# Kernel tuning notes

Hardware: AMD Instinct MI355X
Metric: run time of the kernel (lower is better)

## Reference

```python
import jax, jax.numpy as jnp
import numpy as np

NEG_SLOPE = 0.2  # PyG GATConv default leaky_relu slope


def _gat_layer(h, mask, W, att_src, att_dst, bias, concat):
    """PyG-style GATConv (eval mode, add_self_loops handled via mask diag).
    h: [B,N,D_in], mask: [B,N,N] bool (mask[b,i,j]=True if edge j->i, incl. self loop)
    W: [D_in, H*C], att_src/att_dst: [H,C], bias: [H*C] or [C].
    """
    B, N, _ = h.shape
    H, C = att_src.shape
    x = (h @ W).reshape(B, N, H, C)                       # [B,N,H,C]
    e_src = jnp.einsum('bnhc,hc->bnh', x, att_src)        # score contrib of source j
    e_dst = jnp.einsum('bnhc,hc->bnh', x, att_dst)        # score contrib of target i
    # scores[b,i,j,h] = leaky_relu(e_dst_i + e_src_j)
    s = jax.nn.leaky_relu(e_dst[:, :, None, :] + e_src[:, None, :, :], NEG_SLOPE)
    s = jnp.where(mask[..., None], s, -jnp.inf)
    alpha = jax.nn.softmax(s, axis=2)                     # softmax over neighbors j
    out = jnp.einsum('bijh,bjhc->bihc', alpha, x)         # aggregate
    out = out.reshape(B, N, H * C) if concat else out.mean(axis=2)
    return out + bias


def setup_inputs() -> dict:
    key = jax.random.key(0)
    ks = jax.random.split(key, 16)
    B, T, N, F_in = 4, 8, 2000, 158
    D, H = 128, 4
    C = D // H  # 32
    x_alpha = jax.random.normal(ks[0], (B, T, N, F_in), dtype=jnp.float32)
    sector_graph = (jax.random.uniform(ks[1], (B, N, N)) > 0.98).astype(jnp.float32)
    g = lambda k, shp, fan: jax.random.normal(k, shp, dtype=jnp.float32) / np.sqrt(fan)
    return {
        'x_alpha': x_alpha,
        'sector_graph': sector_graph,
        'W_in': g(ks[2], (F_in, D), F_in), 'b_in': jnp.zeros((D,), jnp.float32),
        'ln_g': jnp.ones((D,), jnp.float32), 'ln_b': jnp.zeros((D,), jnp.float32),
        'W0': g(ks[3], (D, H * C), D), 'as0': g(ks[4], (H, C), C), 'ad0': g(ks[5], (H, C), C),
        'bias0': jnp.zeros((H * C,), jnp.float32),
        'W1': g(ks[6], (D, H * C), D), 'as1': g(ks[7], (H, C), C), 'ad1': g(ks[8], (H, C), C),
        'bias1': jnp.zeros((C,), jnp.float32),
        'W_out': g(ks[9], (C, D), C), 'b_out': jnp.zeros((D,), jnp.float32),
    }


def reference(x_alpha, sector_graph, W_in, b_in, ln_g, ln_b,
              W0, as0, ad0, bias0, W1, as1, ad1, bias1, W_out, b_out):
    B, T, N, _ = x_alpha.shape
    x = x_alpha[:, -1]                                    # [B,N,F]
    # input_proj: Linear -> LayerNorm -> ReLU (dropout is identity in eval)
    h = x @ W_in + b_in
    mu = h.mean(-1, keepdims=True)
    var = ((h - mu) ** 2).mean(-1, keepdims=True)
    h = (h - mu) / jnp.sqrt(var + 1e-5) * ln_g + ln_b
    h = jax.nn.relu(h)                                    # [B,N,128]
    # edge mask with self loops (PyG add_self_loops=True)
    eye = jnp.eye(N, dtype=bool)
    mask = (sector_graph > 0) | eye[None]
    # layer 0: concat=True, out dim 128 == in dim -> residual, elu (not last layer)
    h0 = _gat_layer(h, mask, W0, as0, ad0, bias0, concat=True)
    h = h + jax.nn.elu(h0)
    # layer 1 (last): concat=False, out dim 32 != 128 -> no residual, no elu
    h = _gat_layer(h, mask, W1, as1, ad1, bias1, concat=False)  # [B,N,32]
    return h @ W_out + b_out                              # [B,N,128]
```

## Files before the change

kernel.cpp:

```cpp
#include <hip/hip_runtime.h>

typedef unsigned short u16;

__device__ __forceinline__ float us2f(u16 u){
  unsigned int x = ((unsigned int)u) << 16;
  return __uint_as_float(x);
}
__device__ __forceinline__ u16 f2us(float f){
  unsigned int u = __float_as_uint(f);
  unsigned int r = (u + 0x7fffu + ((u >> 16) & 1u)) >> 16;
  return (u16)r;
}
__device__ __forceinline__ float wredSum(float v){
  #pragma unroll
  for (int o = 32; o > 0; o >>= 1) v += __shfl_xor(v, o, 64);
  return v;
}
__device__ __forceinline__ float g32Sum(float v){
  #pragma unroll
  for (int o = 16; o > 0; o >>= 1) v += __shfl_xor(v, o, 32);
  return v;
}
__device__ __forceinline__ float g8Sum(float v){
  #pragma unroll
  for (int o = 4; o > 0; o >>= 1) v += __shfl_xor(v, o, 32);
  return v;
}

#define ACAP 128
#define RBG 32

__global__ __launch_bounds__(256) void k_inln_gat0(
    const float* __restrict__ xA, const float* __restrict__ Win,
    const float* __restrict__ bin, const float* __restrict__ lng,
    const float* __restrict__ lnb, const float* __restrict__ W0,
    const float* __restrict__ as0, const float* __restrict__ ad0,
    float* __restrict__ h, u16* __restrict__ x0,
    float* __restrict__ es, float* __restrict__ ed)
{
  __shared__ float xs[RBG][160];
  __shared__ float Wt[2][8][128];
  const int t = threadIdx.x;
  const int row0 = blockIdx.x * RBG;
  const int tx = t & 31, ty = t >> 5;
  const int c0 = tx * 4, rbase = ty * 4;
  const int wk = ty;

  for (int idx = t; idx < RBG * 160; idx += 256){
    int r = idx / 160, k = idx - r * 160;
    int row = row0 + r;
    int b = row / 2000, n = row - b * 2000;
    xs[r][k] = (k < 158) ? xA[(((size_t)b * 8 + 7) * 2000 + n) * 158 + k] : 0.f;
  }
  *(float4*)&Wt[0][wk][c0] = *(const float4*)&Win[(size_t)wk * 128 + c0];
  __syncthreads();

  float acc[4][4];
  #pragma unroll
  for (int r = 0; r < 4; r++)
    #pragma unroll
    for (int c = 0; c < 4; c++) acc[r][c] = 0.f;

  const int NT1 = 20;
  for (int tl = 0; tl < NT1; tl++){
    const int cur = tl & 1;
    float4 wreg = make_float4(0.f, 0.f, 0.f, 0.f);
    const bool hn = (tl + 1 < NT1);
    if (hn){
      int k = (tl + 1) * 8 + wk;
      if (k < 158) wreg = *(const float4*)&Win[(size_t)k * 128 + c0];
    }
    const int k0 = tl * 8;
    #pragma unroll
    for (int kh = 0; kh < 2; kh++){
      float4 a[4];
      #pragma unroll
      for (int r = 0; r < 4; r++) a[r] = *(const float4*)&xs[rbase + r][k0 + kh * 4];
      #pragma unroll
      for (int kk = 0; kk < 4; kk++){
        float4 w = *(const float4*)&Wt[cur][kh * 4 + kk][c0];
        #pragma unroll
        for (int r = 0; r < 4; r++){
          float av = ((const float*)&a[r])[kk];
          acc[r][0] = fmaf(av, w.x, acc[r][0]);
          acc[r][1] = fmaf(av, w.y, acc[r][1]);
          acc[r][2] = fmaf(av, w.z, acc[r][2]);
          acc[r][3] = fmaf(av, w.w, acc[r][3]);
        }
      }
    }
    if (hn) *(float4*)&Wt[cur ^ 1][wk][c0] = wreg;
    __syncthreads();
  }

  {
    float4 bi = *(const float4*)&bin[c0];
    float4 g  = *(const float4*)&lng[c0];
    float4 be = *(const float4*)&lnb[c0];
    #pragma unroll
    for (int r = 0; r < 4; r++){
      float a0 = acc[r][0] + bi.x, a1 = acc[r][1] + bi.y;
      float a2 = acc[r][2] + bi.z, a3 = acc[r][3] + bi.w;
      float s  = g32Sum(a0 + a1 + a2 + a3);
      float sq = g32Sum(a0*a0 + a1*a1 + a2*a2 + a3*a3);
      float mu  = s * (1.f / 128.f);
      float var = sq * (1.f / 128.f) - mu * mu;
      float inv = rsqrtf(var + 1e-5f);
      float v0 = fmaxf((a0 - mu) * inv * g.x + be.x, 0.f);
      float v1 = fmaxf((a1 - mu) * inv * g.y + be.y, 0.f);
      float v2 = fmaxf((a2 - mu) * inv * g.z + be.z, 0.f);
      float v3 = fmaxf((a3 - mu) * inv * g.w + be.w, 0.f);
      *(float4*)&xs[rbase + r][c0] = make_float4(v0, v1, v2, v3);
      *(float4*)&h[(size_t)(row0 + rbase + r) * 128 + c0] = make_float4(v0, v1, v2, v3);
    }
  }
  *(float4*)&Wt[0][wk][c0] = *(const float4*)&W0[(size_t)wk * 128 + c0];
  __syncthreads();

  #pragma unroll
  for (int r = 0; r < 4; r++)
    #pragma unroll
    for (int c = 0; c < 4; c++) acc[r][c] = 0.f;
  const int NT2 = 16;
  for (int tl = 0; tl < NT2; tl++){
    const int cur = tl & 1;
    float4 wreg = make_float4(0.f, 0.f, 0.f, 0.f);
    const bool hn = (tl + 1 < NT2);
    if (hn) wreg = *(const float4*)&W0[(size_t)((tl + 1) * 8 + wk) * 128 + c0];
    const int k0 = tl * 8;
    #pragma unroll
    for (int kh = 0; kh < 2; kh++){
      float4 a[4];
      #pragma unroll
      for (int r = 0; r < 4; r++) a[r] = *(const float4*)&xs[rbase + r][k0 + kh * 4];
      #pragma unroll
      for (int kk = 0; kk < 4; kk++){
        float4 w = *(const float4*)&Wt[cur][kh * 4 + kk][c0];
        #pragma unroll
        for (int r = 0; r < 4; r++){
          float av = ((const float*)&a[r])[kk];
          acc[r][0] = fmaf(av, w.x, acc[r][0]);
          acc[r][1] = fmaf(av, w.y, acc[r][1]);
          acc[r][2] = fmaf(av, w.z, acc[r][2]);
          acc[r][3] = fmaf(av, w.w, acc[r][3]);
        }
      }
    }
    if (hn) *(float4*)&Wt[cur ^ 1][wk][c0] = wreg;
    __syncthreads();
  }

  {
    float4 av = *(const float4*)&as0[c0];
    float4 dv = *(const float4*)&ad0[c0];
    const int hh = tx >> 3;
    #pragma unroll
    for (int r = 0; r < 4; r++){
      ushort4 o;
      o.x = f2us(acc[r][0]); o.y = f2us(acc[r][1]);
      o.z = f2us(acc[r][2]); o.w = f2us(acc[r][3]);
      *(ushort4*)(x0 + (size_t)(row0 + rbase + r) * 128 + c0) = o;
      float ps = acc[r][0]*av.x + acc[r][1]*av.y + acc[r][2]*av.z + acc[r][3]*av.w;
      float pd = acc[r][0]*dv.x + acc[r][1]*dv.y + acc[r][2]*dv.z + acc[r][3]*dv.w;
      ps = g8Sum(ps); pd = g8Sum(pd);
      if ((tx & 7) == 0){
        es[(size_t)(row0 + rbase + r) * 4 + hh] = ps;
        ed[(size_t)(row0 + rbase + r) * 4 + hh] = pd;
      }
    }
  }
}

__global__ __launch_bounds__(256) void k_gat_pre(
    const float* __restrict__ hin, const float* __restrict__ W,
    const float* __restrict__ asv, const float* __restrict__ adv,
    u16* __restrict__ x0, float* __restrict__ es, float* __restrict__ ed)
{
  __shared__ float xs[RBG][128];
  __shared__ float Wt[2][8][128];
  const int t = threadIdx.x;
  const int row0 = blockIdx.x * RBG;
  const int tx = t & 31, ty = t >> 5;
  const int c0 = tx * 4, rbase = ty * 4;
  const int wk = ty;

  for (int f = t; f < RBG * 32; f += 256){
    int r = f >> 5, cq = (f & 31) * 4;
    *(float4*)&xs[r][cq] = *(const float4*)&hin[(size_t)(row0 + r) * 128 + cq];
  }
  *(float4*)&Wt[0][wk][c0] = *(const float4*)&W[(size_t)wk * 128 + c0];
  __syncthreads();

  float acc[4][4];
  #pragma unroll
  for (int r = 0; r < 4; r++)
    #pragma unroll
    for (int c = 0; c < 4; c++) acc[r][c] = 0.f;

  const int NT = 16;
  for (int tl = 0; tl < NT; tl++){
    const int cur = tl & 1;
    float4 wreg = make_float4(0.f, 0.f, 0.f, 0.f);
    const bool hn = (tl + 1 < NT);
    if (hn) wreg = *(const float4*)&W[(size_t)((tl + 1) * 8 + wk) * 128 + c0];
    const int k0 = tl * 8;
    #pragma unroll
    for (int kh = 0; kh < 2; kh++){
      float4 a[4];
      #pragma unroll
      for (int r = 0; r < 4; r++) a[r] = *(const float4*)&xs[rbase + r][k0 + kh * 4];
      #pragma unroll
      for (int kk = 0; kk < 4; kk++){
        float4 w = *(const float4*)&Wt[cur][kh * 4 + kk][c0];
        #pragma unroll
        for (int r = 0; r < 4; r++){
          float av = ((const float*)&a[r])[kk];
          acc[r][0] = fmaf(av, w.x, acc[r][0]);
          acc[r][1] = fmaf(av, w.y, acc[r][1]);
          acc[r][2] = fmaf(av, w.z, acc[r][2]);
          acc[r][3] = fmaf(av, w.w, acc[r][3]);
        }
      }
    }
    if (hn) *(float4*)&Wt[cur ^ 1][wk][c0] = wreg;
    __syncthreads();
  }

  {
    float4 av = *(const float4*)&asv[c0];
    float4 dv = *(const float4*)&adv[c0];
    const int hh = tx >> 3;
    #pragma unroll
    for (int r = 0; r < 4; r++){
      ushort4 o;
      o.x = f2us(acc[r][0]); o.y = f2us(acc[r][1]);
      o.z = f2us(acc[r][2]); o.w = f2us(acc[r][3]);
      *(ushort4*)(x0 + (size_t)(row0 + rbase + r) * 128 + c0) = o;
      float ps = acc[r][0]*av.x + acc[r][1]*av.y + acc[r][2]*av.z + acc[r][3]*av.w;
      float pd = acc[r][0]*dv.x + acc[r][1]*dv.y + acc[r][2]*dv.z + acc[r][3]*dv.w;
      ps = g8Sum(ps); pd = g8Sum(pd);
      if ((tx & 7) == 0){
        es[(size_t)(row0 + rbase + r) * 4 + hh] = ps;
        ed[(size_t)(row0 + rbase + r) * 4 + hh] = pd;
      }
    }
  }
}

template<int LAYER>
__global__ __launch_bounds__(256) void k_attn(
    const float* __restrict__ sg,
    u16* __restrict__ adj, int* __restrict__ cnt,
    const u16* __restrict__ x0,
    const float* __restrict__ es, const float* __restrict__ ed,
    const float* __restrict__ bias, float* __restrict__ hio,
    const float* __restrict__ Wout, const float* __restrict__ bout,
    float* __restrict__ outv)
{
  __shared__ int   idx_s[4][ACAP];
  __shared__ float sc[4][4][132];
  const int t = threadIdx.x;
  const int w = t >> 6;
  const int l = t & 63;
  const int bi = blockIdx.x * 4 + w;
  const int b = bi / 2000;
  const int i = bi - b * 2000;

  int m;
  if (LAYER == 0){
    int cloc = 0;
    const float4* row4 = (const float4*)(sg + (size_t)bi * 2000);
    for (int q = 0; q < 8; q++){
      int f4 = q * 64 + l;
      float4 v = make_float4(0.f, 0.f, 0.f, 0.f);
      if (f4 < 500) v = row4[f4];
      #pragma unroll
      for (int u = 0; u < 4; u++){
        int j = f4 * 4 + u;
        bool hit = (f4 < 500) && (((&v.x)[u] > 0.f) || (j == i));
        unsigned long long mask = __ballot(hit);
        if (hit){
          int pos = cloc + (int)__popcll(mask & ((1ull << l) - 1ull));
          if (pos < ACAP){
            idx_s[w][pos] = j;
            adj[(size_t)bi * ACAP + pos] = (u16)j;
          }
        }
        cloc += (int)__popcll(mask);
      }
    }
    if (l == 0) cnt[bi] = min(cloc, ACAP);
    m = min(cloc, ACAP);
  } else {
    m = min(cnt[bi], ACAP);
    if (l < m)      idx_s[w][l]      = (int)adj[(size_t)bi * ACAP + l];
    if (64 + l < m) idx_s[w][64 + l] = (int)adj[(size_t)bi * ACAP + 64 + l];
  }

  float4 edv = *(const float4*)&ed[(size_t)bi * 4];
  float q0 = 0.f, q1 = 0.f, q2 = 0.f, q3 = 0.f;
  #pragma unroll
  for (int rep = 0; rep < 2; rep++){
    int e = rep * 64 + l;
    if (e < m){
      int j = idx_s[w][e];
      float4 esv = *(const float4*)&es[((size_t)b * 2000 + j) * 4];
      float s0 = edv.x + esv.x; s0 = s0 > 0.f ? s0 : 0.2f * s0;
      float s1 = edv.y + esv.y; s1 = s1 > 0.f ? s1 : 0.2f * s1;
      float s2 = edv.z + esv.z; s2 = s2 > 0.f ? s2 : 0.2f * s2;
      float s3 = edv.w + esv.w; s3 = s3 > 0.f ? s3 : 0.2f * s3;
      float p0 = __expf(s0), p1 = __expf(s1), p2 = __expf(s2), p3 = __expf(s3);
      sc[w][0][e] = p0; sc[w][1][e] = p1; sc[w][2][e] = p2; sc[w][3][e] = p3;
      q0 += p0; q1 += p1; q2 += p2; q3 += p3;
    }
  }
  q0 = wredSum(q0); q1 = wredSum(q1); q2 = wredSum(q2); q3 = wredSum(q3);

  const int hh = l >> 4;
  float qh = hh < 2 ? (hh == 0 ? q0 : q1) : (hh == 2 ? q2 : q3);
  float inv = 1.f / qh;
  float a0 = 0.f, a1 = 0.f;
  const u16* x0b = x0 + (size_t)b * 2000 * 128 + 2 * l;
  #pragma unroll 8
  for (int e = 0; e < m; e++){
    float p = sc[w][hh][e];
    int j = idx_s[w][e];
    unsigned int pk = *(const unsigned int*)(x0b + (size_t)j * 128);
    a0 = fmaf(p, us2f((u16)(pk & 0xffffu)), a0);
    a1 = fmaf(p, us2f((u16)(pk >> 16)), a1);
  }
  a0 *= inv; a1 *= inv;

  if (LAYER == 0){
    float2 bb = *(const float2*)&bias[2 * l];
    float v0 = a0 + bb.x; v0 = v0 > 0.f ? v0 : (__expf(v0) - 1.f);
    float v1 = a1 + bb.y; v1 = v1 > 0.f ? v1 : (__expf(v1) - 1.f);
    float2* hp = (float2*)&hio[(size_t)bi * 128 + 2 * l];
    float2 ho = *hp;
    *hp = make_float2(ho.x + v0, ho.y + v1);
  } else {
    float s0 = a0 + __shfl_xor(a0, 16); s0 += __shfl_xor(s0, 32);
    float s1 = a1 + __shfl_xor(a1, 16); s1 += __shfl_xor(s1, 32);
    float mv0 = s0 * 0.25f, mv1 = s1 * 0.25f;
    if (l < 16){
      float2 bb = *(const float2*)&bias[2 * l];
      mv0 += bb.x; mv1 += bb.y;
    }
    float2 bo = *(const float2*)&bout[2 * l];
    float o0 = bo.x, o1 = bo.y;
    #pragma unroll
    for (int p = 0; p < 16; p++){
      float mk0 = __shfl(mv0, p);
      float mk1 = __shfl(mv1, p);
      float2 w0 = *(const float2*)&Wout[(size_t)(2 * p) * 128 + 2 * l];
      float2 w1 = *(const float2*)&Wout[(size_t)(2 * p + 1) * 128 + 2 * l];
      o0 = fmaf(mk0, w0.x, o0); o1 = fmaf(mk0, w0.y, o1);
      o0 = fmaf(mk1, w1.x, o0); o1 = fmaf(mk1, w1.y, o1);
    }
    *(float2*)&outv[(size_t)bi * 128 + 2 * l] = make_float2(o0, o1);
  }
}

extern "C" void kernel_launch(void* const* d_in, const int* in_sizes, int n_in,
                              void* d_out, int out_size, void* d_ws, size_t ws_size,
                              hipStream_t stream) {
  const float* xA   = (const float*)d_in[0];
  const float* sg   = (const float*)d_in[1];
  const float* Win  = (const float*)d_in[2];
  const float* bin  = (const float*)d_in[3];
  const float* lng  = (const float*)d_in[4];
  const float* lnb  = (const float*)d_in[5];
  const float* W0   = (const float*)d_in[6];
  const float* as0  = (const float*)d_in[7];
  const float* ad0  = (const float*)d_in[8];
  const float* b0   = (const float*)d_in[9];
  const float* W1   = (const float*)d_in[10];
  const float* as1  = (const float*)d_in[11];
  const float* ad1  = (const float*)d_in[12];
  const float* b1   = (const float*)d_in[13];
  const float* Wout = (const float*)d_in[14];
  const float* bout = (const float*)d_in[15];

  char* ws = (char*)d_ws;
  float* h    = (float*)(ws);
  u16*   x0   = (u16*)  (ws + 4096000);
  float* es   = (float*)(ws + 6144000);
  float* ed   = (float*)(ws + 6272000);
  u16*   adj  = (u16*)  (ws + 6400000);
  int*   cnt  = (int*)  (ws + 8448000);

  k_inln_gat0 <<<250, 256, 0, stream>>>(xA, Win, bin, lng, lnb, W0, as0, ad0, h, x0, es, ed);
  k_attn<0>   <<<2000, 256, 0, stream>>>(sg, adj, cnt, x0, es, ed, b0, h, nullptr, nullptr, nullptr);
  k_gat_pre   <<<250, 256, 0, stream>>>(h, W1, as1, ad1, x0, es, ed);
  k_attn<1>   <<<2000, 256, 0, stream>>>(nullptr, adj, cnt, x0, es, ed, b1, nullptr, Wout, bout, (float*)d_out);
}
```

Baseline: 200.0 us.

## Move adjacency compaction into input-projection kernel as extra blocks

```diff
diff --git a/kernel.cpp b/kernel.cpp
--- a/kernel.cpp
+++ b/kernel.cpp
@@ -35,12 +35,44 @@
     const float* __restrict__ bin, const float* __restrict__ lng,
     const float* __restrict__ lnb, const float* __restrict__ W0,
     const float* __restrict__ as0, const float* __restrict__ ad0,
+    const float* __restrict__ sg, u16* __restrict__ adj, int* __restrict__ cnt,
     float* __restrict__ h, u16* __restrict__ x0,
     float* __restrict__ es, float* __restrict__ ed)
 {
+  const int t = threadIdx.x;
+
+  if (blockIdx.x >= 250){
+    const int sb = blockIdx.x - 250;
+    const int w = t >> 6, l = t & 63;
+    #pragma unroll
+    for (int rr = 0; rr < 4; rr++){
+      const int bi = sb * 16 + w * 4 + rr;
+      const int b = bi / 2000, i = bi - b * 2000;
+      const float4* row4 = (const float4*)(sg + (size_t)bi * 2000);
+      int cloc = 0;
+      for (int q = 0; q < 8; q++){
+        int f4 = q * 64 + l;
+        float4 v = make_float4(0.f, 0.f, 0.f, 0.f);
+        if (f4 < 500) v = row4[f4];
+        #pragma unroll
+        for (int u = 0; u < 4; u++){
+          int j = f4 * 4 + u;
+          bool hit = (f4 < 500) && (((&v.x)[u] > 0.f) || (j == i));
+          unsigned long long mask = __ballot(hit);
+          if (hit){
+            int pos = cloc + (int)__popcll(mask & ((1ull << l) - 1ull));
+            if (pos < ACAP) adj[(size_t)bi * ACAP + pos] = (u16)j;
+          }
+          cloc += (int)__popcll(mask);
+        }
+      }
+      if (l == 0) cnt[bi] = min(cloc, ACAP);
+    }
+    return;
+  }
+
   __shared__ float xs[RBG][160];
   __shared__ float Wt[2][8][128];
-  const int t = threadIdx.x;
   const int row0 = blockIdx.x * RBG;
   const int tx = t & 31, ty = t >> 5;
   const int c0 = tx * 4, rbase = ty * 4;
@@ -249,8 +281,7 @@
 
 template<int LAYER>
 __global__ __launch_bounds__(256) void k_attn(
-    const float* __restrict__ sg,
-    u16* __restrict__ adj, int* __restrict__ cnt,
+    const u16* __restrict__ adj, const int* __restrict__ cnt,
     const u16* __restrict__ x0,
     const float* __restrict__ es, const float* __restrict__ ed,
     const float* __restrict__ bias, float* __restrict__ hio,
@@ -264,37 +295,12 @@
   const int l = t & 63;
   const int bi = blockIdx.x * 4 + w;
   const int b = bi / 2000;
-  const int i = bi - b * 2000;
-
-  int m;
-  if (LAYER == 0){
-    int cloc = 0;
-    const float4* row4 = (const float4*)(sg + (size_t)bi * 2000);
-    for (int q = 0; q < 8; q++){
-      int f4 = q * 64 + l;
-      float4 v = make_float4(0.f, 0.f, 0.f, 0.f);
-      if (f4 < 500) v = row4[f4];
-      #pragma unroll
-      for (int u = 0; u < 4; u++){
-        int j = f4 * 4 + u;
-        bool hit = (f4 < 500) && (((&v.x)[u] > 0.f) || (j == i));
-        unsigned long long mask = __ballot(hit);
-        if (hit){
-          int pos = cloc + (int)__popcll(mask & ((1ull << l) - 1ull));
-          if (pos < ACAP){
-            idx_s[w][pos] = j;
-            adj[(size_t)bi * ACAP + pos] = (u16)j;
-          }
-        }
-        cloc += (int)__popcll(mask);
-      }
-    }
-    if (l == 0) cnt[bi] = min(cloc, ACAP);
-    m = min(cloc, ACAP);
-  } else {
-    m = min(cnt[bi], ACAP);
-    if (l < m)      idx_s[w][l]      = (int)adj[(size_t)bi * ACAP + l];
-    if (64 + l < m) idx_s[w][64 + l] = (int)adj[(size_t)bi * ACAP + 64 + l];
+
+  const int m = min(cnt[bi], ACAP);
+  {
+    unsigned int pk = *(const unsigned int*)&adj[(size_t)bi * ACAP + 2 * l];
+    if (2 * l < m)     idx_s[w][2 * l]     = (int)(pk & 0xffffu);
+    if (2 * l + 1 < m) idx_s[w][2 * l + 1] = (int)(pk >> 16);
   }
 
   float4 edv = *(const float4*)&ed[(size_t)bi * 4];
@@ -389,8 +395,9 @@
   u16*   adj  = (u16*)  (ws + 6400000);
   int*   cnt  = (int*)  (ws + 8448000);
 
-  k_inln_gat0 <<<250, 256, 0, stream>>>(xA, Win, bin, lng, lnb, W0, as0, ad0, h, x0, es, ed);
-  k_attn<0>   <<<2000, 256, 0, stream>>>(sg, adj, cnt, x0, es, ed, b0, h, nullptr, nullptr, nullptr);
+  k_inln_gat0 <<<750, 256, 0, stream>>>(xA, Win, bin, lng, lnb, W0, as0, ad0,
+                                        sg, adj, cnt, h, x0, es, ed);
+  k_attn<0>   <<<2000, 256, 0, stream>>>(adj, cnt, x0, es, ed, b0, h, nullptr, nullptr, nullptr);
   k_gat_pre   <<<250, 256, 0, stream>>>(h, W1, as1, ad1, x0, es, ed);
-  k_attn<1>   <<<2000, 256, 0, stream>>>(nullptr, adj, cnt, x0, es, ed, b1, nullptr, Wout, bout, (float*)d_out);
-}
+  k_attn<1>   <<<2000, 256, 0, stream>>>(adj, cnt, x0, es, ed, b1, nullptr, Wout, bout, (float*)d_out);
+}
```

Measured after the change: 200.8 us. About the same (+0.4%).
